# Optimization experiments

Measured on AMD Instinct MI355X. Metric: run time of the kernel, lower is better.

Reference implementation:

```python
import jax, jax.numpy as jnp
import numpy as np

DEPTH = 5  # init kwarg


def setup_inputs() -> dict:
    key = jax.random.key(0)
    ks = jax.random.split(key, 10)
    n_atoms, n_bonds, hidden, n_mols = 80000, 160001, 448, 4000
    ATOM_DIM, BOND_DIM = 38, 11
    inp = {
        "fatoms": jax.random.normal(ks[0], (n_atoms, ATOM_DIM), jnp.float32),
        "fbonds": jax.random.normal(ks[1], (n_bonds, ATOM_DIM + BOND_DIM), jnp.float32),
        "W_i": jax.random.normal(ks[2], (ATOM_DIM + BOND_DIM, hidden), jnp.float32) * 0.1,
        "W_h": jax.random.normal(ks[3], (hidden, hidden), jnp.float32) * 0.05,
        "W_o": jax.random.normal(ks[4], (ATOM_DIM + hidden, hidden), jnp.float32) * 0.05,
        "b_o": jax.random.normal(ks[5], (hidden,), jnp.float32),
        "agraph": jax.random.randint(ks[6], (n_atoms, 6), 0, n_bonds, jnp.int64),
        "bgraph": jax.random.randint(ks[7], (n_bonds, 6), 0, n_bonds, jnp.int64),
        "mol_idx": jnp.sort(jax.random.randint(ks[8], (n_atoms,), 0, n_mols, jnp.int64)),
        "n_mols": n_mols,
    }
    return inp


def reference(fatoms, fbonds, W_i, W_h, W_o, b_o, agraph, bgraph, mol_idx, n_mols):
    # binput: [n_bonds, hidden]
    binput = fbonds @ W_i
    message = jax.nn.relu(binput)
    for _ in range(DEPTH - 1):
        # padded-neighbor gather-sum over MAX_NB=6, then linear + relu
        nei = jnp.take(message, bgraph, axis=0).sum(axis=1)  # [n_bonds, hidden]
        message = jax.nn.relu(binput + nei @ W_h)
    # atom readout
    nei = jnp.take(message, agraph, axis=0).sum(axis=1)  # [n_atoms, hidden]
    ainput = jnp.concatenate([fatoms, nei], axis=1)
    atom_hiddens = jax.nn.relu(ainput @ W_o + b_o)
    # per-molecule mean pooling (scope -> segment ids)
    sums = jax.ops.segment_sum(atom_hiddens, mol_idx, num_segments=n_mols)
    counts = jax.ops.segment_sum(jnp.ones((atom_hiddens.shape[0],), atom_hiddens.dtype), mol_idx, num_segments=n_mols)
    return sums / jnp.maximum(counts, 1.0)[:, None]
```

## Files before the change

### kernel.cpp

```cpp
#include <hip/hip_runtime.h>

#define HIDDEN 448

typedef __attribute__((ext_vector_type(8))) short short8;
typedef __attribute__((ext_vector_type(4))) float f32x4;

__device__ __forceinline__ unsigned short f2bf(float f) {
    unsigned int u = __float_as_uint(f);
    u = (u + 0x7fffu + ((u >> 16) & 1u)) >> 16;
    return (unsigned short)u;
}
__device__ __forceinline__ float bf2f(unsigned short h) {
    return __uint_as_float(((unsigned int)h) << 16);
}
__device__ __forceinline__ unsigned int cvt_pk_bf16(float a, float b) {
    unsigned int r;
    asm("v_cvt_pk_bf16_f32 %0, %1, %2" : "=v"(r) : "v"(a), "v"(b));
    return r;
}
__device__ __forceinline__ void async16(void* lds, const void* g) {
    __builtin_amdgcn_global_load_lds(
        (const __attribute__((address_space(1))) unsigned int*)g,
        (__attribute__((address_space(3))) unsigned int*)lds, 16, 0, 0);
}

__global__ __launch_bounds__(256) void prep_wcat_kernel(
    const float* __restrict__ Wtop, int Ktop, const float* __restrict__ Wbot,
    unsigned short* __restrict__ out)
{
    const int idx = blockIdx.x * 256 + threadIdx.x;
    if (idx >= 448 * 512) return;
    const int n = idx >> 9, k = idx & 511;
    float v = 0.0f;
    if (k < Ktop) v = Wtop[k * HIDDEN + n];
    else if (k >= 64) v = Wbot[(k - 64) * HIDDEN + n];
    out[(size_t)n * 512 + (k ^ ((n & 3) << 3))] = f2bf(v);
}

__global__ __launch_bounds__(256) void prep_apad_kernel(
    const float* __restrict__ A, int K, unsigned short* __restrict__ out,
    int Mreal, int total)
{
    const int idx = blockIdx.x * 256 + threadIdx.x;
    if (idx >= total) return;
    const int row = idx >> 6, k = idx & 63;
    const float v = (row < Mreal && k < K) ? A[(size_t)row * K + k] : 0.0f;
    out[(size_t)row * 64 + (k ^ ((row & 3) << 3))] = f2bf(v);
}

template<int OUTQ>
__global__ __launch_bounds__(512, 4) void gemm_mfma_kernel(
    const unsigned short* __restrict__ Apad,
    const unsigned short* A2,
    const unsigned short* __restrict__ BT,
    const float* __restrict__ bias,
    unsigned short* outh,
    unsigned char* __restrict__ outq,
    float* __restrict__ outs,
    int M, int nsteps)
{
    __shared__ __align__(16) unsigned char smem[33792];
    unsigned short* As = (unsigned short*)smem;
    unsigned short* Bs = (unsigned short*)(smem + 4096);
    float* rmaxbuf = (float*)(smem + 32768);

    const int tid = threadIdx.x, lane = tid & 63, wv = tid >> 6;
    const int row0 = blockIdx.x * 64;
    const int wrow = (wv & 1) * 32;
    const int wcol = (wv >> 1) * 112;
    const int rr = lane & 15, ch = lane >> 4;
    const int lrow = lane >> 2, lq = lane & 3;

    f32x4 acc[2][7] = {};

    for (int s = 0; s < nsteps; ++s) {
        #pragma unroll
        for (int i = 0; i < 4; ++i) {
            const int t = wv + 8 * i;
            if (t < 28)
                async16(Bs + t * 512 + lane * 8,
                        BT + (size_t)(t * 16 + lrow) * 512 + s * 32 + lq * 8);
        }
        if (wv >= 4) {
            const int a = wv - 4;
            const int grow = row0 + a * 16 + lrow;
            const unsigned short* src = (s < 2)
                ? Apad + (size_t)grow * 64 + s * 32 + lq * 8
                : A2 + (size_t)grow * HIDDEN + (s - 2) * 32 + lq * 8;
            async16(As + a * 512 + lane * 8, src);
        }
        __syncthreads();

        short8 av[2];
        #pragma unroll
        for (int m = 0; m < 2; ++m) {
            const int r = wrow + m * 16 + rr;
            av[m] = *(const short8*)&As[r * 32 + ((ch ^ (r & 3)) << 3)];
        }
        #pragma unroll
        for (int n = 0; n < 7; ++n) {
            const int cl = wcol + n * 16 + rr;
            const short8 bv = *(const short8*)&Bs[cl * 32 + ((ch ^ (cl & 3)) << 3)];
            #pragma unroll
            for (int m = 0; m < 2; ++m)
                acc[m][n] = __builtin_amdgcn_mfma_f32_16x16x32_bf16(
                    av[m], bv, acc[m][n], 0, 0, 0);
        }
        __syncthreads();
    }

    const int r4 = ch << 2;

    if (OUTQ) {
        float rpm[2][4];
        #pragma unroll
        for (int m = 0; m < 2; ++m)
            #pragma unroll
            for (int j = 0; j < 4; ++j) {
                float mx = 0.0f;
                #pragma unroll
                for (int n = 0; n < 7; ++n) mx = fmaxf(mx, acc[m][n][j]);
                rpm[m][j] = mx;
            }
        #pragma unroll
        for (int off = 1; off < 16; off <<= 1)
            #pragma unroll
            for (int m = 0; m < 2; ++m)
                #pragma unroll
                for (int j = 0; j < 4; ++j)
                    rpm[m][j] = fmaxf(rpm[m][j], __shfl_xor(rpm[m][j], off));
        if (rr == 0)
            #pragma unroll
            for (int m = 0; m < 2; ++m)
                #pragma unroll
                for (int j = 0; j < 4; ++j)
                    rmaxbuf[(wrow + m * 16 + r4 + j) * 4 + (wv >> 1)] = rpm[m][j];
        __syncthreads();
        float inv[2][4];
        #pragma unroll
        for (int m = 0; m < 2; ++m)
            #pragma unroll
            for (int j = 0; j < 4; ++j) {
                const int rl = wrow + m * 16 + r4 + j;
                const float mx = fmaxf(fmaxf(rmaxbuf[rl * 4 + 0], rmaxbuf[rl * 4 + 1]),
                                       fmaxf(rmaxbuf[rl * 4 + 2], rmaxbuf[rl * 4 + 3]));
                inv[m][j] = (mx > 0.0f) ? (255.0f / mx) : 0.0f;
                if (wv < 2 && rr == 0 && row0 + rl < M)
                    outs[row0 + rl] = mx * (1.0f / 255.0f);
            }
        unsigned char* q8 = smem;
        #pragma unroll
        for (int m = 0; m < 2; ++m)
            #pragma unroll
            for (int j = 0; j < 4; ++j) {
                const int rl = wrow + m * 16 + r4 + j;
                #pragma unroll
                for (int n = 0; n < 7; ++n) {
                    const float v = fmaxf(acc[m][n][j], 0.0f);
                    q8[rl * 448 + wcol + n * 16 + rr] =
                        (unsigned char)__float2uint_rn(fminf(v * inv[m][j], 255.0f));
                }
            }
        __syncthreads();
        #pragma unroll
        for (int i = 0; i < 4; ++i) {
            const int u = tid + 512 * i;
            if (u < 1792 && row0 + u / 28 < M)
                ((uint4*)(outq + (size_t)row0 * 448))[u] = ((const uint4*)q8)[u];
        }
    } else {
        #pragma unroll
        for (int n = 0; n < 7; ++n) {
            const int col = wcol + n * 16 + rr;
            const float bsv = bias ? bias[col] : 0.0f;
            #pragma unroll
            for (int m = 0; m < 2; ++m)
                #pragma unroll
                for (int j = 0; j < 4; ++j) {
                    const int row = row0 + wrow + m * 16 + r4 + j;
                    if (row < M)
                        outh[(size_t)row * HIDDEN + col] =
                            f2bf(fmaxf(acc[m][n][j] + bsv, 0.0f));
                }
        }
    }
}

__global__ __launch_bounds__(256) void gather_deq_kernel(
    const unsigned char* __restrict__ Xq, const float* __restrict__ Xs,
    const int* __restrict__ graph,
    unsigned short* __restrict__ nei, int M)
{
    const int row = blockIdx.x * 4 + (threadIdx.x >> 6);
    const int lane = threadIdx.x & 63;
    if (row >= M || lane >= 56) return;
    const int* g = graph + (size_t)row * 6;
    float acc[8] = {};
    #pragma unroll
    for (int j = 0; j < 6; ++j) {
        const int gj = g[j];
        const float s = Xs[gj];
        const uint2 b = *((const uint2*)(Xq + (size_t)gj * HIDDEN) + lane);
        acc[0] += (float)(b.x & 255u) * s;
        acc[1] += (float)((b.x >> 8) & 255u) * s;
        acc[2] += (float)((b.x >> 16) & 255u) * s;
        acc[3] += (float)(b.x >> 24) * s;
        acc[4] += (float)(b.y & 255u) * s;
        acc[5] += (float)((b.y >> 8) & 255u) * s;
        acc[6] += (float)((b.y >> 16) & 255u) * s;
        acc[7] += (float)(b.y >> 24) * s;
    }
    uint4 o;
    o.x = cvt_pk_bf16(acc[0], acc[1]);
    o.y = cvt_pk_bf16(acc[2], acc[3]);
    o.z = cvt_pk_bf16(acc[4], acc[5]);
    o.w = cvt_pk_bf16(acc[6], acc[7]);
    const int c = lane ^ (row & 3);
    *((uint4*)(nei + (size_t)row * HIDDEN) + c) = o;
}

__global__ void segmean_kernel(
    const unsigned short* __restrict__ ah, const int* __restrict__ mol_idx,
    float* __restrict__ out, int n_atoms)
{
    const int m = blockIdx.x;
    const int c = threadIdx.x;
    int l = 0, r = n_atoms;
    while (l < r) { const int mid = (l + r) >> 1; if (mol_idx[mid] < m) l = mid + 1; else r = mid; }
    const int start = l;
    r = n_atoms;
    while (l < r) { const int mid = (l + r) >> 1; if (mol_idx[mid] < m + 1) l = mid + 1; else r = mid; }
    const int end = l;
    float acc = 0.0f;
    for (int a = start; a < end; ++a) acc += bf2f(ah[(size_t)a * HIDDEN + c]);
    out[(size_t)m * HIDDEN + c] = acc / fmaxf((float)(end - start), 1.0f);
}

__global__ __launch_bounds__(256) void fill_kernel(float* __restrict__ out, int n, float val)
{
    const int i = blockIdx.x * 256 + threadIdx.x;
    if (i < n) out[i] = val;
}

extern "C" void kernel_launch(void* const* d_in, const int* in_sizes, int n_in,
                              void* d_out, int out_size, void* d_ws, size_t ws_size,
                              hipStream_t stream)
{
    const float* fatoms = (const float*)d_in[0];
    const float* fbonds = (const float*)d_in[1];
    const float* W_i    = (const float*)d_in[2];
    const float* W_h    = (const float*)d_in[3];
    const float* W_o    = (const float*)d_in[4];
    const float* b_o    = (const float*)d_in[5];
    const int*   agraph = (const int*)d_in[6];
    const int*   bgraph = (const int*)d_in[7];
    const int*   mol_idx= (const int*)d_in[8];

    const int n_atoms = in_sizes[0] / 38;
    const int n_bonds = in_sizes[1] / 49;
    const int n_mols  = out_size / HIDDEN;

    const int Mb_b = (n_bonds + 63) & ~63;
    const int Mb_a = (n_atoms + 63) & ~63;

    const size_t eW  = (size_t)448 * 512;
    const size_t eFb = (size_t)Mb_b * 64;
    const size_t eFa = (size_t)Mb_a * 64;
    const size_t eX  = (size_t)Mb_b * HIDDEN;

    const size_t need = 2 * eW * 2 + eFb * 2 + eFa * 2 + eX  +
                        (size_t)Mb_b * 4  + eX * 2 ;

    const dim3 blk(256);

    if (ws_size >= need) {
        unsigned short* WhcatT  = (unsigned short*)d_ws;
        unsigned short* WocatT  = WhcatT + eW;
        unsigned short* fbondsP = WocatT + eW;
        unsigned short* fatomsP = fbondsP + eFb;
        unsigned char*  Xq      = (unsigned char*)(fatomsP + eFa);
        float*          Xs      = (float*)(Xq + eX);
        unsigned short* nei     = (unsigned short*)(Xs + Mb_b);

        const int wblocks = (448 * 512 + 255) / 256;
        hipLaunchKernelGGL(prep_wcat_kernel, dim3(wblocks), blk, 0, stream,
                           W_i, 49, W_h, WhcatT);
        hipLaunchKernelGGL(prep_wcat_kernel, dim3(wblocks), blk, 0, stream,
                           W_o, 38, W_o + 38 * HIDDEN, WocatT);
        hipLaunchKernelGGL(prep_apad_kernel, dim3(((int)eFb + 255) / 256), blk, 0, stream,
                           fbonds, 49, fbondsP, n_bonds, (int)eFb);
        hipLaunchKernelGGL(prep_apad_kernel, dim3(((int)eFa + 255) / 256), blk, 0, stream,
                           fatoms, 38, fatomsP, n_atoms, (int)eFa);

        const dim3 gB(Mb_b / 64), gA(Mb_a / 64), tpb(512);

        hipLaunchKernelGGL((gemm_mfma_kernel<1>), gB, tpb, 0, stream,
                           fbondsP, (const unsigned short*)nullptr, WhcatT,
                           (const float*)nullptr, (unsigned short*)nullptr,
                           Xq, Xs, n_bonds, 2);
        for (int it = 0; it < 4; ++it) {
            hipLaunchKernelGGL(gather_deq_kernel, dim3((n_bonds + 3) / 4), blk, 0, stream,
                               Xq, Xs, bgraph, nei, n_bonds);
            hipLaunchKernelGGL((gemm_mfma_kernel<1>), gB, tpb, 0, stream,
                               fbondsP, nei, WhcatT,
                               (const float*)nullptr, (unsigned short*)nullptr,
                               Xq, Xs, n_bonds, 16);
        }
        hipLaunchKernelGGL(gather_deq_kernel, dim3((n_atoms + 3) / 4), blk, 0, stream,
                           Xq, Xs, agraph, nei, n_atoms);
        hipLaunchKernelGGL((gemm_mfma_kernel<0>), gA, tpb, 0, stream,
                           fatomsP, nei, WocatT, b_o, nei,
                           (unsigned char*)nullptr, (float*)nullptr, n_atoms, 16);
        hipLaunchKernelGGL(segmean_kernel, dim3(n_mols), dim3(HIDDEN), 0, stream,
                           nei, mol_idx, (float*)d_out, n_atoms);
    } else {
        const float val = -(float)((double)ws_size / (1024.0 * 1024.0));
        hipLaunchKernelGGL(fill_kernel, dim3((out_size + 255) / 256), blk, 0, stream,
                           (float*)d_out, out_size, val);
    }
}
```

Before: 1.087 ms.

## Change LDS swizzle pattern and write GEMM epilogue outputs directly with lane shuffles

Switches the XOR swizzle for the A and B tiles from row&3 to (row>>1)&3 in every producer and consumer, aiming to cut LDS bank conflicts on the MFMA operand reads. The quantized epilogue no longer stages bytes through shared memory with an extra barrier. It packs four bytes per lane via shuffles and stores them straight to global memory. The bf16 epilogue packs neighbouring columns into 32-bit stores. Row bounds checks are dropped for the quantized output and scale writes, which relies on the buffers being padded to the tile size.

After: 1.156 ms. +6.4%, slower.

```diff
diff --git a/kernel.cpp b/kernel.cpp
--- a/kernel.cpp
+++ b/kernel.cpp
@@ -34,7 +34,7 @@
     float v = 0.0f;
     if (k < Ktop) v = Wtop[k * HIDDEN + n];
     else if (k >= 64) v = Wbot[(k - 64) * HIDDEN + n];
-    out[(size_t)n * 512 + (k ^ ((n & 3) << 3))] = f2bf(v);
+    out[(size_t)n * 512 + (k ^ (((n >> 1) & 3) << 3))] = f2bf(v);
 }
 
 __global__ __launch_bounds__(256) void prep_apad_kernel(
@@ -45,7 +45,7 @@
     if (idx >= total) return;
     const int row = idx >> 6, k = idx & 63;
     const float v = (row < Mreal && k < K) ? A[(size_t)row * K + k] : 0.0f;
-    out[(size_t)row * 64 + (k ^ ((row & 3) << 3))] = f2bf(v);
+    out[(size_t)row * 64 + (k ^ (((row >> 1) & 3) << 3))] = f2bf(v);
 }
 
 template<int OUTQ>
@@ -95,12 +95,12 @@
         #pragma unroll
         for (int m = 0; m < 2; ++m) {
             const int r = wrow + m * 16 + rr;
-            av[m] = *(const short8*)&As[r * 32 + ((ch ^ (r & 3)) << 3)];
+            av[m] = *(const short8*)&As[r * 32 + ((ch ^ ((r >> 1) & 3)) << 3)];
         }
         #pragma unroll
         for (int n = 0; n < 7; ++n) {
             const int cl = wcol + n * 16 + rr;
-            const short8 bv = *(const short8*)&Bs[cl * 32 + ((ch ^ (cl & 3)) << 3)];
+            const short8 bv = *(const short8*)&Bs[cl * 32 + ((ch ^ ((cl >> 1) & 3)) << 3)];
             #pragma unroll
             for (int m = 0; m < 2; ++m)
                 acc[m][n] = __builtin_amdgcn_mfma_f32_16x16x32_bf16(
@@ -136,7 +136,6 @@
                 for (int j = 0; j < 4; ++j)
                     rmaxbuf[(wrow + m * 16 + r4 + j) * 4 + (wv >> 1)] = rpm[m][j];
         __syncthreads();
-        float inv[2][4];
         #pragma unroll
         for (int m = 0; m < 2; ++m)
             #pragma unroll
@@ -144,30 +143,24 @@
                 const int rl = wrow + m * 16 + r4 + j;
                 const float mx = fmaxf(fmaxf(rmaxbuf[rl * 4 + 0], rmaxbuf[rl * 4 + 1]),
                                        fmaxf(rmaxbuf[rl * 4 + 2], rmaxbuf[rl * 4 + 3]));
-                inv[m][j] = (mx > 0.0f) ? (255.0f / mx) : 0.0f;
-                if (wv < 2 && rr == 0 && row0 + rl < M)
+                const float inv = (mx > 0.0f) ? (255.0f / mx) : 0.0f;
+                if (wv < 2 && rr == 0)
                     outs[row0 + rl] = mx * (1.0f / 255.0f);
-            }
-        unsigned char* q8 = smem;
-        #pragma unroll
-        for (int m = 0; m < 2; ++m)
-            #pragma unroll
-            for (int j = 0; j < 4; ++j) {
-                const int rl = wrow + m * 16 + r4 + j;
                 #pragma unroll
                 for (int n = 0; n < 7; ++n) {
                     const float v = fmaxf(acc[m][n][j], 0.0f);
-                    q8[rl * 448 + wcol + n * 16 + rr] =
-                        (unsigned char)__float2uint_rn(fminf(v * inv[m][j], 255.0f));
+                    const unsigned int b0 =
+                        __float2uint_rn(fminf(v * inv, 255.0f));
+                    const unsigned int b1 = __shfl_down(b0, 1);
+                    const unsigned int b2 = __shfl_down(b0, 2);
+                    const unsigned int b3 = __shfl_down(b0, 3);
+                    if ((rr & 3) == 0) {
+                        const unsigned int w = b0 | (b1 << 8) | (b2 << 16) | (b3 << 24);
+                        *(unsigned int*)(outq + (size_t)(row0 + rl) * 448
+                                         + wcol + n * 16 + rr) = w;
+                    }
                 }
             }
-        __syncthreads();
-        #pragma unroll
-        for (int i = 0; i < 4; ++i) {
-            const int u = tid + 512 * i;
-            if (u < 1792 && row0 + u / 28 < M)
-                ((uint4*)(outq + (size_t)row0 * 448))[u] = ((const uint4*)q8)[u];
-        }
     } else {
         #pragma unroll
         for (int n = 0; n < 7; ++n) {
@@ -178,9 +171,11 @@
                 #pragma unroll
                 for (int j = 0; j < 4; ++j) {
                     const int row = row0 + wrow + m * 16 + r4 + j;
-                    if (row < M)
-                        outh[(size_t)row * HIDDEN + col] =
-                            f2bf(fmaxf(acc[m][n][j] + bsv, 0.0f));
+                    const float v = fmaxf(acc[m][n][j] + bsv, 0.0f);
+                    const float vodd = __shfl_down(v, 1);
+                    if (!(rr & 1) && row < M)
+                        *(unsigned int*)(outh + (size_t)row * HIDDEN + col) =
+                            cvt_pk_bf16(v, vodd);
                 }
         }
     }
@@ -215,7 +210,7 @@
     o.y = cvt_pk_bf16(acc[2], acc[3]);
     o.z = cvt_pk_bf16(acc[4], acc[5]);
     o.w = cvt_pk_bf16(acc[6], acc[7]);
-    const int c = lane ^ (row & 3);
+    const int c = lane ^ ((row >> 1) & 3);
     *((uint4*)(nei + (size_t)row * HIDDEN) + c) = o;
 }
 
```

## Fuse neighbor gather-dequant into GEMM A-tile load and double-buffer quantized messages

Applied to the files above, without the earlier changes.

Removes the separate gather_deq kernel and the bf16 nei buffer. Each GEMM block now gathers the six int8 neighbor rows for its own 64 rows, dequantizes and sums them, and writes the bf16 A tile straight into LDS. The quantized message buffers are ping-ponged because the GEMM reads the previous iteration while writing the next. The LDS swizzle changes to use (row>>1)&3 so it matches the new 8-byte per-thread write pattern. This saves a full write and read of the nei tensor plus launches, at the cost of doing scattered gathers inside the GEMM k-loop, which may stall MFMA work.

Result: faster. 968.0 us (-11.0%).

```diff
diff --git a/kernel.cpp b/kernel.cpp
--- a/kernel.cpp
+++ b/kernel.cpp
@@ -34,7 +34,7 @@
     float v = 0.0f;
     if (k < Ktop) v = Wtop[k * HIDDEN + n];
     else if (k >= 64) v = Wbot[(k - 64) * HIDDEN + n];
-    out[(size_t)n * 512 + (k ^ ((n & 3) << 3))] = f2bf(v);
+    out[(size_t)n * 512 + (k ^ (((n >> 1) & 3) << 3))] = f2bf(v);
 }
 
 __global__ __launch_bounds__(256) void prep_apad_kernel(
@@ -45,13 +45,15 @@
     if (idx >= total) return;
     const int row = idx >> 6, k = idx & 63;
     const float v = (row < Mreal && k < K) ? A[(size_t)row * K + k] : 0.0f;
-    out[(size_t)row * 64 + (k ^ ((row & 3) << 3))] = f2bf(v);
-}
-
-template<int OUTQ>
+    out[(size_t)row * 64 + (k ^ (((row >> 1) & 3) << 3))] = f2bf(v);
+}
+
+template<int GRAPH, int OUTQ>
 __global__ __launch_bounds__(512, 4) void gemm_mfma_kernel(
     const unsigned short* __restrict__ Apad,
-    const unsigned short* A2,
+    const unsigned char* __restrict__ Xq,
+    const float* __restrict__ Xs,
+    const int* __restrict__ graph,
     const unsigned short* __restrict__ BT,
     const float* __restrict__ bias,
     unsigned short* outh,
@@ -71,6 +73,21 @@
     const int rr = lane & 15, ch = lane >> 4;
     const int lrow = lane >> 2, lq = lane & 3;
 
+    const int arow = tid >> 3, asub = tid & 7;
+    int goff[6]; float gscl[6];
+    if (GRAPH) {
+        const int grow = row0 + arow;
+        const bool ok = grow < M;
+        #pragma unroll
+        for (int j = 0; j < 6; ++j) {
+            const int gj = ok ? graph[(size_t)grow * 6 + j] : 0;
+            goff[j] = gj * 448;
+            gscl[j] = ok ? Xs[gj] : 0.0f;
+        }
+    }
+    const int awaddr = arow * 32 + (((asub >> 1) ^ ((arow >> 1) & 3)) << 3)
+                     + (asub & 1) * 4;
+
     f32x4 acc[2][7] = {};
 
     for (int s = 0; s < nsteps; ++s) {
@@ -81,13 +98,27 @@
                 async16(Bs + t * 512 + lane * 8,
                         BT + (size_t)(t * 16 + lrow) * 512 + s * 32 + lq * 8);
         }
-        if (wv >= 4) {
-            const int a = wv - 4;
-            const int grow = row0 + a * 16 + lrow;
-            const unsigned short* src = (s < 2)
-                ? Apad + (size_t)grow * 64 + s * 32 + lq * 8
-                : A2 + (size_t)grow * HIDDEN + (s - 2) * 32 + lq * 8;
-            async16(As + a * 512 + lane * 8, src);
+        if (s < 2) {
+            if (wv >= 4) {
+                const int a = wv - 4;
+                const int grow = row0 + a * 16 + lrow;
+                async16(As + a * 512 + lane * 8,
+                        Apad + (size_t)grow * 64 + s * 32 + lq * 8);
+            }
+        } else if (GRAPH) {
+            const int colb = (s - 2) * 32 + asub * 4;
+            float a0 = 0, a1 = 0, a2 = 0, a3 = 0;
+            #pragma unroll
+            for (int j = 0; j < 6; ++j) {
+                const unsigned int b = *(const unsigned int*)(Xq + goff[j] + colb);
+                const float sc = gscl[j];
+                a0 += (float)(b & 255u) * sc;
+                a1 += (float)((b >> 8) & 255u) * sc;
+                a2 += (float)((b >> 16) & 255u) * sc;
+                a3 += (float)(b >> 24) * sc;
+            }
+            *(uint2*)&As[awaddr] = make_uint2(cvt_pk_bf16(a0, a1),
+                                              cvt_pk_bf16(a2, a3));
         }
         __syncthreads();
 
@@ -95,12 +126,12 @@
         #pragma unroll
         for (int m = 0; m < 2; ++m) {
             const int r = wrow + m * 16 + rr;
-            av[m] = *(const short8*)&As[r * 32 + ((ch ^ (r & 3)) << 3)];
+            av[m] = *(const short8*)&As[r * 32 + ((ch ^ ((r >> 1) & 3)) << 3)];
         }
         #pragma unroll
         for (int n = 0; n < 7; ++n) {
             const int cl = wcol + n * 16 + rr;
-            const short8 bv = *(const short8*)&Bs[cl * 32 + ((ch ^ (cl & 3)) << 3)];
+            const short8 bv = *(const short8*)&Bs[cl * 32 + ((ch ^ ((cl >> 1) & 3)) << 3)];
             #pragma unroll
             for (int m = 0; m < 2; ++m)
                 acc[m][n] = __builtin_amdgcn_mfma_f32_16x16x32_bf16(
@@ -184,39 +215,6 @@
                 }
         }
     }
-}
-
-__global__ __launch_bounds__(256) void gather_deq_kernel(
-    const unsigned char* __restrict__ Xq, const float* __restrict__ Xs,
-    const int* __restrict__ graph,
-    unsigned short* __restrict__ nei, int M)
-{
-    const int row = blockIdx.x * 4 + (threadIdx.x >> 6);
-    const int lane = threadIdx.x & 63;
-    if (row >= M || lane >= 56) return;
-    const int* g = graph + (size_t)row * 6;
-    float acc[8] = {};
-    #pragma unroll
-    for (int j = 0; j < 6; ++j) {
-        const int gj = g[j];
-        const float s = Xs[gj];
-        const uint2 b = *((const uint2*)(Xq + (size_t)gj * HIDDEN) + lane);
-        acc[0] += (float)(b.x & 255u) * s;
-        acc[1] += (float)((b.x >> 8) & 255u) * s;
-        acc[2] += (float)((b.x >> 16) & 255u) * s;
-        acc[3] += (float)(b.x >> 24) * s;
-        acc[4] += (float)(b.y & 255u) * s;
-        acc[5] += (float)((b.y >> 8) & 255u) * s;
-        acc[6] += (float)((b.y >> 16) & 255u) * s;
-        acc[7] += (float)(b.y >> 24) * s;
-    }
-    uint4 o;
-    o.x = cvt_pk_bf16(acc[0], acc[1]);
-    o.y = cvt_pk_bf16(acc[2], acc[3]);
-    o.z = cvt_pk_bf16(acc[4], acc[5]);
-    o.w = cvt_pk_bf16(acc[6], acc[7]);
-    const int c = lane ^ (row & 3);
-    *((uint4*)(nei + (size_t)row * HIDDEN) + c) = o;
 }
 
 __global__ void segmean_kernel(
@@ -266,10 +264,10 @@
     const size_t eW  = (size_t)448 * 512;
     const size_t eFb = (size_t)Mb_b * 64;
     const size_t eFa = (size_t)Mb_a * 64;
-    const size_t eX  = (size_t)Mb_b * HIDDEN;
-
-    const size_t need = 2 * eW * 2 + eFb * 2 + eFa * 2 + eX  +
-                        (size_t)Mb_b * 4  + eX * 2 ;
+    const size_t eX  = (size_t)Mb_b * 448;
+
+    const size_t need = 2 * eW * 2 + eFb * 2 + eFa * 2 +
+                        2 * eX + 2 * (size_t)Mb_b * 4;
 
     const dim3 blk(256);
 
@@ -278,9 +276,10 @@
         unsigned short* WocatT  = WhcatT + eW;
         unsigned short* fbondsP = WocatT + eW;
         unsigned short* fatomsP = fbondsP + eFb;
-        unsigned char*  Xq      = (unsigned char*)(fatomsP + eFa);
-        float*          Xs      = (float*)(Xq + eX);
-        unsigned short* nei     = (unsigned short*)(Xs + Mb_b);
+        unsigned char*  Xq0     = (unsigned char*)(fatomsP + eFa);
+        unsigned char*  Xq1     = Xq0 + eX;
+        float*          Xs0     = (float*)(Xq1 + eX);
+        float*          Xs1     = Xs0 + Mb_b;
 
         const int wblocks = (448 * 512 + 255) / 256;
         hipLaunchKernelGGL(prep_wcat_kernel, dim3(wblocks), blk, 0, stream,
@@ -294,25 +293,27 @@
 
         const dim3 gB(Mb_b / 64), gA(Mb_a / 64), tpb(512);
 
-        hipLaunchKernelGGL((gemm_mfma_kernel<1>), gB, tpb, 0, stream,
-                           fbondsP, (const unsigned short*)nullptr, WhcatT,
-                           (const float*)nullptr, (unsigned short*)nullptr,
-                           Xq, Xs, n_bonds, 2);
+        unsigned char* Xq[2] = {Xq0, Xq1};
+        float*         Xs[2] = {Xs0, Xs1};
+
+        hipLaunchKernelGGL((gemm_mfma_kernel<0, 1>), gB, tpb, 0, stream,
+                           fbondsP, (const unsigned char*)nullptr, (const float*)nullptr,
+                           (const int*)nullptr, WhcatT, (const float*)nullptr,
+                           (unsigned short*)nullptr, Xq[0], Xs[0], n_bonds, 2);
+        int p = 0;
         for (int it = 0; it < 4; ++it) {
-            hipLaunchKernelGGL(gather_deq_kernel, dim3((n_bonds + 3) / 4), blk, 0, stream,
-                               Xq, Xs, bgraph, nei, n_bonds);
-            hipLaunchKernelGGL((gemm_mfma_kernel<1>), gB, tpb, 0, stream,
-                               fbondsP, nei, WhcatT,
+            hipLaunchKernelGGL((gemm_mfma_kernel<1, 1>), gB, tpb, 0, stream,
+                               fbondsP, Xq[p], Xs[p], bgraph, WhcatT,
                                (const float*)nullptr, (unsigned short*)nullptr,
-                               Xq, Xs, n_bonds, 16);
-        }
-        hipLaunchKernelGGL(gather_deq_kernel, dim3((n_atoms + 3) / 4), blk, 0, stream,
-                           Xq, Xs, agraph, nei, n_atoms);
-        hipLaunchKernelGGL((gemm_mfma_kernel<0>), gA, tpb, 0, stream,
-                           fatomsP, nei, WocatT, b_o, nei,
-                           (unsigned char*)nullptr, (float*)nullptr, n_atoms, 16);
+                               Xq[p ^ 1], Xs[p ^ 1], n_bonds, 16);
+            p ^= 1;
+        }
+        unsigned short* ah = (unsigned short*)Xq[p ^ 1];
+        hipLaunchKernelGGL((gemm_mfma_kernel<1, 0>), gA, tpb, 0, stream,
+                           fatomsP, Xq[p], Xs[p], agraph, WocatT, b_o,
+                           ah, (unsigned char*)nullptr, (float*)nullptr, n_atoms, 16);
         hipLaunchKernelGGL(segmean_kernel, dim3(n_mols), dim3(HIDDEN), 0, stream,
-                           nei, mol_idx, (float*)d_out, n_atoms);
+                           ah, mol_idx, (float*)d_out, n_atoms);
     } else {
         const float val = -(float)((double)ws_size / (1024.0 * 1024.0));
         hipLaunchKernelGGL(fill_kernel, dim3((out_size + 255) / 256), blk, 0, stream,
```
